# Kernel optimization log

Hardware: AMD Instinct MI355X
Metric: run time of the kernel (lower is better)

The kernel has to match this reference:

```python
import jax, jax.numpy as jnp
import numpy as np

IN_F = 4096
OUT_F = 4096
B, S = 4, 2048


def _quantize_weight(w_float):
    """Replicates Int4PackedLinear.__init__ double quantization; returns reg_b and w_scale."""
    w_amax = jnp.abs(w_float).max()
    scale = jnp.where(w_amax == 0, 1.0, w_amax / 127.0)
    w_int8 = jnp.clip(jnp.round(w_float / scale), -127, 127).astype(jnp.int8)
    low4_amax = jnp.abs(w_int8.astype(jnp.float32)).max()
    low4_scale = jnp.where(low4_amax == 0, 1.0, low4_amax / 7.0)
    w_low = jnp.clip(jnp.round(w_int8.astype(jnp.float32) / low4_scale), -7, 7).astype(jnp.int8)
    w_rec = jnp.round(w_low.astype(jnp.float32) * low4_scale).astype(jnp.int8)
    w_high = jnp.clip(w_int8.astype(jnp.int32) - w_rec.astype(jnp.int32), -7, 7).astype(jnp.int8)
    reg_b = (w_rec.astype(jnp.int32) + w_high.astype(jnp.int32)).astype(jnp.int8)  # w_combined
    return reg_b, scale.astype(jnp.float32)


def setup_inputs() -> dict:
    key = jax.random.key(0)
    k1, k2, k3 = jax.random.split(key, 3)
    w_float = jax.random.normal(k1, (OUT_F, IN_F), dtype=jnp.float32) * 0.02
    reg_b, w_scale = _quantize_weight(w_float)
    x = jax.random.normal(k2, (B, S, IN_F), dtype=jnp.float32)
    bias = jax.random.normal(k3, (OUT_F,), dtype=jnp.float32) * 0.01
    # gate=1.0 >= threshold=0.3 -> full-precision INT8 path uses reg_b
    return {"x": x, "w_int": reg_b, "w_scale": w_scale, "bias": bias}


def reference(x, w_int, w_scale, bias):
    # --- dynamic per-tensor activation quantization ---
    x_amax = jnp.abs(x).max()
    x_scale = jnp.where(x_amax == 0, jnp.float32(1.0), x_amax / 127.0)
    x_int8 = jnp.clip(jnp.round(x / x_scale), -127, 127).astype(jnp.int8)
    # --- integer matmul (accumulate in int32, like torch._int_mm) ---
    out_i32 = jnp.einsum(
        'bsk,nk->bsn',
        x_int8.astype(jnp.int32),
        w_int.astype(jnp.int32),
    )  # [B, S, OUT_F]
    # --- dequant scale in bf16 AFTER the integer matmul, then bias add ---
    combined_scale = (x_scale * w_scale).astype(jnp.bfloat16)
    out = out_i32.astype(jnp.bfloat16) * combined_scale
    out = out + bias  # bf16 + fp32 -> fp32, matching torch promotion
    return out
```

## Files before the change

### kernel.cpp

```cpp
#include <hip/hip_runtime.h>
#include <hip/hip_bf16.h>
#include <stdint.h>

#define IN_F  4096
#define OUT_F 4096
#define BSZ   4
#define SEQ   2048
#define MDIM  (BSZ * SEQ)

typedef __attribute__((address_space(1))) uint8_t ga_u8_t;
typedef __attribute__((address_space(3))) uint8_t ls_u8_t;

__device__ __forceinline__ void gload16_lds(const void* g, void* l) {
    __builtin_amdgcn_global_load_lds((ga_u8_t*)g, (ls_u8_t*)l, 16, 0, 0);
}

__device__ __forceinline__ float bf16_rne(float f) {
    unsigned u = __float_as_uint(f);
    u = (u + 0x7fffu + ((u >> 16) & 1u)) & 0xffff0000u;
    return __uint_as_float(u);
}

__global__ void amax_kernel(const float* __restrict__ x, int n4,
                            unsigned int* __restrict__ amax_u) {
    const float4* x4 = (const float4*)x;
    int idx = blockIdx.x * blockDim.x + threadIdx.x;
    int stride = gridDim.x * blockDim.x;
    float m = 0.0f;
    for (int i = idx; i < n4; i += stride) {
        float4 v = x4[i];
        m = fmaxf(m, fmaxf(fmaxf(fabsf(v.x), fabsf(v.y)),
                           fmaxf(fabsf(v.z), fabsf(v.w))));
    }
    for (int off = 32; off > 0; off >>= 1)
        m = fmaxf(m, __shfl_down(m, off, 64));
    __shared__ float sm[4];
    int lane = threadIdx.x & 63, wave = threadIdx.x >> 6;
    if (lane == 0) sm[wave] = m;
    __syncthreads();
    if (threadIdx.x == 0) {
        m = fmaxf(fmaxf(sm[0], sm[1]), fmaxf(sm[2], sm[3]));
        atomicMax(amax_u, __float_as_uint(m));
    }
}

__global__ void prep_kernel(const float* __restrict__ x,
                            const int* __restrict__ w,
                            signed char* __restrict__ x8,
                            signed char* __restrict__ w8,
                            const unsigned int* __restrict__ amax_u,
                            int nx4, int nw4) {
    int idx = blockIdx.x * blockDim.x + threadIdx.x;
    if (idx < nx4) {
        float amax = __uint_as_float(*amax_u);
        float xs = (amax == 0.0f) ? 1.0f : (amax / 127.0f);
        float4 v = ((const float4*)x)[idx];
        char4 q;
        q.x = (signed char)fminf(fmaxf(rintf(v.x / xs), -127.0f), 127.0f);
        q.y = (signed char)fminf(fmaxf(rintf(v.y / xs), -127.0f), 127.0f);
        q.z = (signed char)fminf(fmaxf(rintf(v.z / xs), -127.0f), 127.0f);
        q.w = (signed char)fminf(fmaxf(rintf(v.w / xs), -127.0f), 127.0f);
        ((char4*)x8)[idx] = q;
    } else {
        int widx = idx - nx4;
        if (widx < nw4) {
            int4 v = ((const int4*)w)[widx];
            char4 q;
            q.x = (signed char)v.x; q.y = (signed char)v.y;
            q.z = (signed char)v.z; q.w = (signed char)v.w;
            ((char4*)w8)[widx] = q;
        }
    }
}

using i32x4 = __attribute__((ext_vector_type(4))) int;

__global__ __launch_bounds__(256, 2) void gemm_i8_kernel(
    const signed char* __restrict__ A,
    const signed char* __restrict__ B,
    const unsigned int* __restrict__ amax_u,
    const float* __restrict__ wscale_p,
    const float* __restrict__ bias,
    float* __restrict__ out) {
    __shared__ signed char sA[128 * 64];
    __shared__ signed char sB[128 * 64];

    const int t = threadIdx.x;
    const int lane = t & 63;
    const int wave = t >> 6;
    const int wm = wave >> 1;
    const int wn = wave & 1;

    const int bid = blockIdx.x;
    const int mt = (bid >> 8) * 8 + (bid & 7);
    const int nt = (bid & 255) >> 3;
    const int tileM = mt * 128;
    const int tileN = nt * 128;

    const int g0 = t, g1 = t + 256;
    const int ar0 = g0 >> 2, ac0 = ((g0 & 3) ^ ((ar0 >> 1) & 3)) * 16;
    const int ar1 = g1 >> 2, ac1 = ((g1 & 3) ^ ((ar1 >> 1) & 3)) * 16;

    const signed char* gA0 = A + (size_t)(tileM + ar0) * IN_F + ac0;
    const signed char* gA1 = A + (size_t)(tileM + ar1) * IN_F + ac1;
    const signed char* gB0 = B + (size_t)(tileN + ar0) * IN_F + ac0;
    const signed char* gB1 = B + (size_t)(tileN + ar1) * IN_F + ac1;

    signed char* lA0 = sA + g0 * 16;
    signed char* lA1 = sA + g1 * 16;
    signed char* lB0 = sB + g0 * 16;
    signed char* lB1 = sB + g1 * 16;

    i32x4 acc[4][4] = {};

    const signed char* aptr[4];
    const signed char* bptr[4];
#pragma unroll
    for (int i = 0; i < 4; ++i) {
        int rowa = wm * 64 + i * 16 + (lane & 15);
        int ca = ((lane >> 4) ^ ((rowa >> 1) & 3)) * 16;
        aptr[i] = sA + rowa * 64 + ca;
        int rowb = wn * 64 + i * 16 + (lane & 15);
        int cb = ((lane >> 4) ^ ((rowb >> 1) & 3)) * 16;
        bptr[i] = sB + rowb * 64 + cb;
    }

    for (int k0 = 0; k0 < IN_F; k0 += 64) {
        __syncthreads();
        gload16_lds(gA0 + k0, lA0);
        gload16_lds(gA1 + k0, lA1);
        gload16_lds(gB0 + k0, lB0);
        gload16_lds(gB1 + k0, lB1);
        __syncthreads();

        i32x4 aF[4], bF[4];
#pragma unroll
        for (int i = 0; i < 4; ++i) aF[i] = *(const i32x4*)aptr[i];
#pragma unroll
        for (int j = 0; j < 4; ++j) bF[j] = *(const i32x4*)bptr[j];
#pragma unroll
        for (int i = 0; i < 4; ++i)
#pragma unroll
            for (int j = 0; j < 4; ++j)
                acc[i][j] = __builtin_amdgcn_mfma_i32_16x16x64_i8(
                    aF[i], bF[j], acc[i][j], 0, 0, 0);
    }

    float amax = __uint_as_float(*amax_u);
    float xs = (amax == 0.0f) ? 1.0f : (amax / 127.0f);
    float cs = bf16_rne(xs * wscale_p[0]);

#pragma unroll
    for (int j = 0; j < 4; ++j) {
        int n = tileN + wn * 64 + j * 16 + (lane & 15);
        float bz = bias[n];
#pragma unroll
        for (int i = 0; i < 4; ++i) {
            int row0 = tileM + wm * 64 + i * 16 + (lane >> 4) * 4;
#pragma unroll
            for (int r = 0; r < 4; ++r) {
                float v = bf16_rne((float)acc[i][j][r]);
                float p = bf16_rne(v * cs);
                __builtin_nontemporal_store(
                    p + bz, &out[(size_t)(row0 + r) * OUT_F + n]);
            }
        }
    }
}

extern "C" void kernel_launch(void* const* d_in, const int* in_sizes, int n_in,
                              void* d_out, int out_size, void* d_ws,
                              size_t ws_size, hipStream_t stream) {
    const float* x = (const float*)d_in[0];
    const int* w_int = (const int*)d_in[1];
    const float* w_scale = (const float*)d_in[2];
    const float* bias = (const float*)d_in[3];
    float* out = (float*)d_out;

    unsigned char* ws = (unsigned char*)d_ws;
    unsigned int* amax_u = (unsigned int*)ws;
    signed char* w8 = (signed char*)(ws + 64);
    signed char* x8 = (signed char*)(ws + 64 + (size_t)OUT_F * IN_F);

    hipMemsetAsync(amax_u, 0, 4, stream);

    const int n_x4 = MDIM * IN_F / 4;
    const int n_w4 = OUT_F * IN_F / 4;

    amax_kernel<<<4096, 256, 0, stream>>>(x, n_x4, amax_u);
    prep_kernel<<<(n_x4 + n_w4) / 256, 256, 0, stream>>>(
        x, w_int, x8, w8, amax_u, n_x4, n_w4);

    const int nblocks = (MDIM / 128) * (OUT_F / 128);
    gemm_i8_kernel<<<nblocks, 256, 0, stream>>>(x8, w8, amax_u, w_scale, bias,
                                                out);
}
```

Before: 466.6 us.

## Rewrite int8 GEMM as 256x256 tile with triple-buffered LDS pipeline

The GEMM goes from 128x128 tiles with 4 waves and a synchronous load-then-compute loop to 256x256 tiles with 8 waves. Global-to-LDS loads run through a 3-stage ring buffer, prefetching two k-tiles ahead, with manual vmcnt waits and barriers. MFMA work is split into four phases interleaved with the staged loads, and s_setprio raises priority during the MFMA bursts. The aim is to hide global load latency, raise arithmetic intensity per LDS byte, and cut barrier stalls. In exchange it uses 96KB of LDS and 128 accumulator registers per thread, which limits occupancy, and it launches only 512 workgroups.

```diff
diff --git a/kernel.cpp b/kernel.cpp
--- a/kernel.cpp
+++ b/kernel.cpp
@@ -75,76 +75,128 @@
 
 using i32x4 = __attribute__((ext_vector_type(4))) int;
 
-__global__ __launch_bounds__(256, 2) void gemm_i8_kernel(
+#define FENCE() asm volatile("" ::: "memory")
+#define BAR()   do { FENCE(); __builtin_amdgcn_s_barrier(); FENCE(); } while (0)
+#define WAITV4() asm volatile("s_waitcnt vmcnt(4)" ::: "memory")
+#define WAITV0() asm volatile("s_waitcnt vmcnt(0)" ::: "memory")
+#define WAITL0() asm volatile("s_waitcnt lgkmcnt(0)" ::: "memory")
+
+#define MFMA8(P)                                                             \
+    _Pragma("unroll")                                                        \
+    for (int j = 0; j < 4; ++j) {                                            \
+        acc[2*(P)][j]   = __builtin_amdgcn_mfma_i32_16x16x64_i8(             \
+            aX, bF[j], acc[2*(P)][j], 0, 0, 0);                              \
+        acc[2*(P)+1][j] = __builtin_amdgcn_mfma_i32_16x16x64_i8(             \
+            aY, bF[j], acc[2*(P)+1][j], 0, 0, 0);                            \
+    }
+
+#define PHASE_TAIL(P)                                                        \
+    BAR();                                                                   \
+    WAITL0();                                                                \
+    __builtin_amdgcn_sched_barrier(0);                                       \
+    __builtin_amdgcn_s_setprio(1);                                           \
+    MFMA8(P);                                                                \
+    __builtin_amdgcn_s_setprio(0);                                           \
+    BAR();
+
+#define TILE(T, DOSTAGE, TW3)                                                \
+    {                                                                        \
+        const signed char* base = smem + ((T) % 3) * 32768;                  \
+        signed char* sbase = smem + (((T) + 2) % 3) * 32768;                 \
+        const int kst = ((T) + 2) * 64;                                      \
+                                      \
+        bF[0] = *(const i32x4*)(base + boff[0]);                             \
+        bF[1] = *(const i32x4*)(base + boff[1]);                             \
+        bF[2] = *(const i32x4*)(base + boff[2]);                             \
+        bF[3] = *(const i32x4*)(base + boff[3]);                             \
+        aX = *(const i32x4*)(base + aoff[0]);                                \
+        aY = *(const i32x4*)(base + aoff[1]);                                \
+        if (DOSTAGE) gload16_lds(gA0 + kst, sbase + dA0);                    \
+        PHASE_TAIL(0)                                                        \
+                                                                \
+        aX = *(const i32x4*)(base + aoff[2]);                                \
+        aY = *(const i32x4*)(base + aoff[3]);                                \
+        if (DOSTAGE) gload16_lds(gA1 + kst, sbase + dA1);                    \
+        PHASE_TAIL(1)                                                        \
+                                                                \
+        aX = *(const i32x4*)(base + aoff[4]);                                \
+        aY = *(const i32x4*)(base + aoff[5]);                                \
+        if (DOSTAGE) gload16_lds(gB0 + kst, sbase + dB0);                    \
+        PHASE_TAIL(2)                                                        \
+                                                                \
+        aX = *(const i32x4*)(base + aoff[6]);                                \
+        aY = *(const i32x4*)(base + aoff[7]);                                \
+        if (DOSTAGE) gload16_lds(gB1 + kst, sbase + dB1);                    \
+        TW3;                                                                 \
+        PHASE_TAIL(3)                                                        \
+    }
+
+__global__ __launch_bounds__(512, 2) void gemm_i8_kernel(
     const signed char* __restrict__ A,
     const signed char* __restrict__ B,
     const unsigned int* __restrict__ amax_u,
     const float* __restrict__ wscale_p,
     const float* __restrict__ bias,
     float* __restrict__ out) {
-    __shared__ signed char sA[128 * 64];
-    __shared__ signed char sB[128 * 64];
-
-    const int t = threadIdx.x;
-    const int lane = t & 63;
-    const int wave = t >> 6;
-    const int wm = wave >> 1;
-    const int wn = wave & 1;
+    __shared__ signed char smem[3 * 32768];
+
+    const int tid = threadIdx.x;
+    const int lane = tid & 63;
+    const int wave = tid >> 6;
+    const int wm = wave >> 2;
+    const int wn = wave & 3;
 
     const int bid = blockIdx.x;
-    const int mt = (bid >> 8) * 8 + (bid & 7);
-    const int nt = (bid & 255) >> 3;
-    const int tileM = mt * 128;
-    const int tileN = nt * 128;
-
-    const int g0 = t, g1 = t + 256;
-    const int ar0 = g0 >> 2, ac0 = ((g0 & 3) ^ ((ar0 >> 1) & 3)) * 16;
-    const int ar1 = g1 >> 2, ac1 = ((g1 & 3) ^ ((ar1 >> 1) & 3)) * 16;
-
-    const signed char* gA0 = A + (size_t)(tileM + ar0) * IN_F + ac0;
-    const signed char* gA1 = A + (size_t)(tileM + ar1) * IN_F + ac1;
-    const signed char* gB0 = B + (size_t)(tileN + ar0) * IN_F + ac0;
-    const signed char* gB1 = B + (size_t)(tileN + ar1) * IN_F + ac1;
-
-    signed char* lA0 = sA + g0 * 16;
-    signed char* lA1 = sA + g1 * 16;
-    signed char* lB0 = sB + g0 * 16;
-    signed char* lB1 = sB + g1 * 16;
-
-    i32x4 acc[4][4] = {};
-
-    const signed char* aptr[4];
-    const signed char* bptr[4];
-#pragma unroll
-    for (int i = 0; i < 4; ++i) {
-        int rowa = wm * 64 + i * 16 + (lane & 15);
-        int ca = ((lane >> 4) ^ ((rowa >> 1) & 3)) * 16;
-        aptr[i] = sA + rowa * 64 + ca;
-        int rowb = wn * 64 + i * 16 + (lane & 15);
-        int cb = ((lane >> 4) ^ ((rowb >> 1) & 3)) * 16;
-        bptr[i] = sB + rowb * 64 + cb;
-    }
-
-    for (int k0 = 0; k0 < IN_F; k0 += 64) {
-        __syncthreads();
-        gload16_lds(gA0 + k0, lA0);
-        gload16_lds(gA1 + k0, lA1);
-        gload16_lds(gB0 + k0, lB0);
-        gload16_lds(gB1 + k0, lB1);
-        __syncthreads();
-
-        i32x4 aF[4], bF[4];
-#pragma unroll
-        for (int i = 0; i < 4; ++i) aF[i] = *(const i32x4*)aptr[i];
-#pragma unroll
-        for (int j = 0; j < 4; ++j) bF[j] = *(const i32x4*)bptr[j];
-#pragma unroll
-        for (int i = 0; i < 4; ++i)
-#pragma unroll
-            for (int j = 0; j < 4; ++j)
-                acc[i][j] = __builtin_amdgcn_mfma_i32_16x16x64_i8(
-                    aF[i], bF[j], acc[i][j], 0, 0, 0);
-    }
+    const int wg = (bid & 7) * 64 + (bid >> 3);
+    const int mt = wg >> 4;
+    const int nt = wg & 15;
+    const int tileM = mt * 256;
+    const int tileN = nt * 256;
+
+    const int g = tid;
+    const int srow = g >> 2;
+    const int scol = ((g & 3) ^ ((srow >> 1) & 3)) * 16;
+    const signed char* gA0 = A + (size_t)(tileM +       srow) * IN_F + scol;
+    const signed char* gA1 = A + (size_t)(tileM + 128 + srow) * IN_F + scol;
+    const signed char* gB0 = B + (size_t)(tileN +       srow) * IN_F + scol;
+    const signed char* gB1 = B + (size_t)(tileN + 128 + srow) * IN_F + scol;
+    const int dA0 = g * 16;
+    const int dA1 = 8192  + g * 16;
+    const int dB0 = 16384 + g * 16;
+    const int dB1 = 24576 + g * 16;
+
+    int aoff[8], boff[4];
+    const int kc = lane >> 4;
+#pragma unroll
+    for (int i = 0; i < 8; ++i) {
+        int r = wm * 128 + i * 16 + (lane & 15);
+        aoff[i] = r * 64 + ((kc ^ ((r >> 1) & 3)) * 16);
+    }
+#pragma unroll
+    for (int j = 0; j < 4; ++j) {
+        int r = wn * 64 + j * 16 + (lane & 15);
+        boff[j] = 16384 + r * 64 + ((kc ^ ((r >> 1) & 3)) * 16);
+    }
+
+    i32x4 acc[8][4] = {};
+    i32x4 bF[4], aX, aY;
+
+    gload16_lds(gA0,      smem + dA0);
+    gload16_lds(gA1,      smem + dA1);
+    gload16_lds(gB0,      smem + dB0);
+    gload16_lds(gB1,      smem + dB1);
+    gload16_lds(gA0 + 64, smem + 32768 + dA0);
+    gload16_lds(gA1 + 64, smem + 32768 + dA1);
+    gload16_lds(gB0 + 64, smem + 32768 + dB0);
+    gload16_lds(gB1 + 64, smem + 32768 + dB1);
+    WAITV4();
+    BAR();
+
+    for (int kt = 0; kt < 62; ++kt) {
+        TILE(kt, true, WAITV4());
+    }
+    TILE(62, false, WAITV0());
+    TILE(63, false, (void)0);
 
     float amax = __uint_as_float(*amax_u);
     float xs = (amax == 0.0f) ? 1.0f : (amax / 127.0f);
@@ -155,8 +207,8 @@
         int n = tileN + wn * 64 + j * 16 + (lane & 15);
         float bz = bias[n];
 #pragma unroll
-        for (int i = 0; i < 4; ++i) {
-            int row0 = tileM + wm * 64 + i * 16 + (lane >> 4) * 4;
+        for (int i = 0; i < 8; ++i) {
+            int row0 = tileM + wm * 128 + i * 16 + (lane >> 4) * 4;
 #pragma unroll
             for (int r = 0; r < 4; ++r) {
                 float v = bf16_rne((float)acc[i][j][r]);
@@ -191,7 +243,7 @@
     prep_kernel<<<(n_x4 + n_w4) / 256, 256, 0, stream>>>(
         x, w_int, x8, w8, amax_u, n_x4, n_w4);
 
-    const int nblocks = (MDIM / 128) * (OUT_F / 128);
-    gemm_i8_kernel<<<nblocks, 256, 0, stream>>>(x8, w8, amax_u, w_scale, bias,
+    const int nblocks = (MDIM / 256) * (OUT_F / 256);
+    gemm_i8_kernel<<<nblocks, 512, 0, stream>>>(x8, w8, amax_u, w_scale, bias,
                                                 out);
 }
```

New measurement: 427.4 us. 1.09x faster.
